# Kernel tuning notes

Measured on AMD Instinct MI355X. Metric: run time of the kernel, lower is better.

## Reference

```python
import jax, jax.numpy as jnp
import numpy as np

SCALE = 0.5

def setup_inputs() -> dict:
    key = jax.random.key(0)
    kx, kw, kb = jax.random.split(key, 3)
    N, Cin, H, W = 32, 64, 128, 128
    Cout, K = 128, 3
    x = jax.random.normal(kx, (N, Cin, H, W), dtype=jnp.float32)
    # kaiming_uniform with a=sqrt(5) -> bound = sqrt(3/fan_in) approx; uniform is fine for a reference
    fan_in = Cin * K * K
    bound = 1.0 / np.sqrt(fan_in)
    weight = jax.random.uniform(kw, (Cout, Cin, K, K), dtype=jnp.float32, minval=-bound, maxval=bound)
    bias = jax.random.uniform(kb, (Cout,), dtype=jnp.float32, minval=-bound, maxval=bound)
    return {"x": x, "weight": weight, "bias": bias}

def reference(x, weight, bias):
    # valid conv, stride 1: (N, Cout, OH, OW)
    y = jax.lax.conv_general_dilated(
        x, weight,
        window_strides=(1, 1),
        padding="VALID",
        dimension_numbers=("NCHW", "OIHW", "NCHW"),
    )
    y = (y + bias[None, :, None, None]) * SCALE
    # min over output channels, keepdim -> (N, 1, OH, OW)
    return jnp.min(y, axis=1, keepdims=True)
```

## Files before the change

kernel.cpp:

```cpp
#include <hip/hip_runtime.h>

constexpr int CN   = 32;
constexpr int CIN  = 64;
constexpr int CH   = 128;
constexpr int CW   = 128;
constexpr int COUT = 128;
constexpr int OHh  = 126;
constexpr int OWw  = 126;
constexpr int KTOT = 576;

typedef __attribute__((ext_vector_type(8))) short bf16x8;
typedef __attribute__((ext_vector_type(4))) float f32x4;

__device__ __forceinline__ unsigned short f2bf(float f) {
  union { float f; unsigned u; } v; v.f = f;
  unsigned u = v.u;
  u += 0x7FFFu + ((u >> 16) & 1u);
  return (unsigned short)(u >> 16);
}

__device__ __forceinline__ void gload_lds16(const unsigned short* g, unsigned short* l) {
  __builtin_amdgcn_global_load_lds(
      (const __attribute__((address_space(1))) unsigned int*)g,
      (__attribute__((address_space(3))) unsigned int*)l, 16, 0, 0);
}

__global__ __launch_bounds__(256) void prep_xt_kernel(const float* __restrict__ x,
                                                      unsigned short* __restrict__ xt) {
  __shared__ __align__(16) unsigned short s[128][72];
  const int b = blockIdx.x;
  const int n = b >> 7, h = b & 127;
  const float* src = x + (size_t)n * CIN * CH * CW + (size_t)h * CW;
  const int t = threadIdx.x;
  #pragma unroll
  for (int r = 0; r < 8; ++r) {
    int idx = r * 256 + t;
    int ci = idx >> 5, c0 = (idx & 31) << 2;
    float4 v = *(const float4*)(src + (size_t)ci * (CH * CW) + c0);
    s[c0 + 0][ci] = f2bf(v.x);
    s[c0 + 1][ci] = f2bf(v.y);
    s[c0 + 2][ci] = f2bf(v.z);
    s[c0 + 3][ci] = f2bf(v.w);
  }
  __syncthreads();
  unsigned short* dst = xt + (size_t)b * 8192;
  #pragma unroll
  for (int r = 0; r < 4; ++r) {
    int idx = r * 256 + t;
    int c = idx >> 3, sl = idx & 7;
    int half = sl >> 2, q = sl & 3;
    int lo = q ^ ((c >> 1) & 3);
    uint4 v = *(const uint4*)&s[c][half * 32 + lo * 8];
    *(uint4*)(dst + (size_t)c * 64 + sl * 8) = v;
  }
}

__global__ void prep_wt2_kernel(const float* __restrict__ w,
                                unsigned short* __restrict__ wt) {
  int i = blockIdx.x * 256 + threadIdx.x;
  if (i >= COUT * KTOT) return;
  int co = i / KTOT, k = i - co * KTOT;
  int kw = k / 192, r = k - kw * 192;
  int kh = r >> 6, q = r & 63;
  int half = q >> 5, qq = q & 31;
  int sl = qq >> 3, j = qq & 7;
  int o = sl ^ ((co >> 1) & 3);
  int ci = half * 32 + o * 8 + j;
  wt[i] = f2bf(w[co * 576 + ci * 9 + kh * 3 + kw]);
}

__global__ __launch_bounds__(512, 2)
void conv_min_mfma4(const unsigned short* __restrict__ xt,
                    const unsigned short* __restrict__ wt,
                    const float* __restrict__ bias,
                    float* __restrict__ out) {
  __shared__ __align__(16) unsigned short sX[2][4][132][32];
  __shared__ __align__(16) unsigned short sW[2][3][128][32];
  __shared__ float sRed[2][512];

  const int t   = threadIdx.x;
  const int bid = blockIdx.x;
  const int swz = (bid & 7) * 128 + (bid >> 3);
  const int n   = swz >> 5;
  const int oh0 = (swz & 31) * 4;

  const int lane = t & 63, w = t >> 6;
  const int wc = w & 1, wp = w >> 1;
  const int lg = lane >> 4, ln = lane & 15;

  const int xcq   = (t >> 2) * 64 + (t & 3) * 8;
  const int wco_o = (t >> 2) * 576 + (t & 3) * 8;

  const int chA = lg ^ ((ln >> 1) & 3);
  const char* Abase = (const char*)&sW[0][0][0][0] +
                      ((wc * 64 + ln) * 64 + chA * 16);
  const char* Bbase[3];
  #pragma unroll
  for (int kw = 0; kw < 3; ++kw) {
    int chB = lg ^ (((ln + kw) >> 1) & 3);
    Bbase[kw] = (const char*)&sX[0][0][0][0] +
                (wp * 8448 + (ln + kw) * 64 + chB * 16);
  }

  f32x4 acc[4][8];
  #pragma unroll
  for (int i = 0; i < 4; ++i)
    #pragma unroll
    for (int j = 0; j < 8; ++j)
      acc[i][j] = (f32x4){0.f, 0.f, 0.f, 0.f};

  auto stage = [&](int g, int bf) {
    const int kh = g >> 1, half = g & 1;
    unsigned short* ldsX = &sX[bf][0][0][0];
    unsigned short* ldsW = &sW[bf][0][0][0];
    #pragma unroll
    for (int r = 0; r < 4; ++r) {
      int h = oh0 + kh + r;
      h = h > 127 ? 127 : h;
      gload_lds16(xt + ((size_t)(n * 128 + h) << 13) + half * 32 + xcq,
                  ldsX + r * 4224 + w * 512);
    }
    const int wb = kh * 64 + half * 32;
    #pragma unroll
    for (int r = 0; r < 3; ++r)
      gload_lds16(wt + wb + wco_o + r * 192,
                  ldsW + r * 4096 + w * 512);
  };

  stage(0, 0);
  #pragma unroll
  for (int g = 0; g < 6; ++g) {
    const int bf = g & 1;
    if (g < 5) {
      stage(g + 1, bf ^ 1);
      __builtin_amdgcn_sched_barrier(0);
      asm volatile("s_waitcnt vmcnt(7)" ::: "memory");
    } else {
      asm volatile("s_waitcnt vmcnt(0)" ::: "memory");
    }
    __builtin_amdgcn_s_barrier();
    __builtin_amdgcn_sched_barrier(0);
    #pragma unroll
    for (int kw = 0; kw < 3; ++kw) {
      bf16x8 af[4], bfr[8];
      #pragma unroll
      for (int mi = 0; mi < 4; ++mi)
        af[mi] = *(const bf16x8*)(Abase + bf * 24576 + kw * 8192 + mi * 1024);
      #pragma unroll
      for (int ni = 0; ni < 8; ++ni)
        bfr[ni] = *(const bf16x8*)(Bbase[kw] + bf * 33792 + ni * 1024);
      #pragma unroll
      for (int mi = 0; mi < 4; ++mi)
        #pragma unroll
        for (int ni = 0; ni < 8; ++ni)
          acc[mi][ni] = __builtin_amdgcn_mfma_f32_16x16x32_bf16(
              af[mi], bfr[ni], acc[mi][ni], 0, 0, 0);
    }
    __builtin_amdgcn_s_barrier();
  }

  float bv[4][4];
  #pragma unroll
  for (int mi = 0; mi < 4; ++mi)
    #pragma unroll
    for (int r = 0; r < 4; ++r)
      bv[mi][r] = bias[wc * 64 + mi * 16 + lg * 4 + r];

  #pragma unroll
  for (int ni = 0; ni < 8; ++ni) {
    float m = 3.4e38f;
    #pragma unroll
    for (int mi = 0; mi < 4; ++mi)
      #pragma unroll
      for (int r = 0; r < 4; ++r)
        m = fminf(m, (acc[mi][ni][r] + bv[mi][r]) * 0.5f);
    m = fminf(m, __shfl_xor(m, 16));
    m = fminf(m, __shfl_xor(m, 32));
    if (lg == 0) sRed[wc][wp * 128 + ni * 16 + ln] = m;
  }
  __syncthreads();
  {
    int row = t >> 7, c = t & 127;
    if (c < OWw && oh0 + row < OHh)
      out[((size_t)n * OHh + oh0 + row) * OWw + c] = fminf(sRed[0][t], sRed[1][t]);
  }
}

__global__ void prep_wt_kernel(const float* __restrict__ w,
                               unsigned short* __restrict__ wt) {
  int i = blockIdx.x * 256 + threadIdx.x;
  if (i >= COUT * KTOT) return;
  int co = i / KTOT, kp = i - co * KTOT;
  int kw = kp / 192, rem = kp - kw * 192;
  int ci = rem / 3, kh = rem - ci * 3;
  wt[i] = f2bf(w[co * 576 + ci * 9 + kh * 3 + kw]);
}

template <bool USE_WT>
__global__ __launch_bounds__(256, 2)
void conv_min_fb(const float* __restrict__ x, const float* __restrict__ w,
                 const float* __restrict__ bias, const unsigned short* __restrict__ wt,
                 float* __restrict__ out) {
  __shared__ __align__(16) unsigned short sW[128][40];
  __shared__ __align__(16) unsigned short sX[128][40];
  __shared__ float sBias[COUT];
  __shared__ float sRed[2][128];
  const int t = threadIdx.x, bid = blockIdx.x;
  const int n = bid / OHh, oh = bid - n * OHh;
  if (t < COUT) sBias[t] = bias[t];
  const int hq = t & 7, q = t >> 3, c0 = q * 4;
  const int wco = t >> 1, whalf = t & 1;
  const int lane = t & 63, lg = lane >> 4, ln = lane & 15;
  const int wv = t >> 6, wc = wv & 1, wp = wv >> 1;
  f32x4 acc[4][4];
  #pragma unroll
  for (int i = 0; i < 4; ++i)
    #pragma unroll
    for (int j = 0; j < 4; ++j) acc[i][j] = (f32x4){0.f, 0.f, 0.f, 0.f};
  const float* xn = x + (size_t)n * CIN * CH * CW;
  for (int s = 0; s < 18; ++s) {
    const int k0 = s * 32;
    const int kw_s = s / 6;
    const int rembase = (s - kw_s * 6) * 32;
    float4 xa[2], xb[2]; int kkp[2];
    #pragma unroll
    for (int pi = 0; pi < 2; ++pi) {
      const int kk = 2 * hq + 16 * pi; kkp[pi] = kk;
      int rem0 = rembase + kk, ci0 = rem0 / 3, kh0 = rem0 - ci0 * 3;
      int rem1 = rem0 + 1, ci1 = rem1 / 3, kh1 = rem1 - ci1 * 3;
      xa[pi] = *(const float4*)(xn + (ci0 * CH + (oh + kh0)) * CW + c0);
      xb[pi] = *(const float4*)(xn + (ci1 * CH + (oh + kh1)) * CW + c0);
    }
    uint4 wv0, wv1;
    if constexpr (USE_WT) {
      const uint4* src = (const uint4*)(wt + wco * KTOT + k0 + whalf * 16);
      wv0 = src[0]; wv1 = src[1];
    } else {
      unsigned tmp[8];
      #pragma unroll
      for (int e = 0; e < 8; ++e) {
        int kk = whalf * 16 + 2 * e;
        int rem0 = rembase + kk, ci0 = rem0 / 3, kh0 = rem0 - ci0 * 3;
        int rem1 = rem0 + 1, ci1 = rem1 / 3, kh1 = rem1 - ci1 * 3;
        tmp[e] = (unsigned)f2bf(w[wco * 576 + ci0 * 9 + kh0 * 3 + kw_s]) |
                 ((unsigned)f2bf(w[wco * 576 + ci1 * 9 + kh1 * 3 + kw_s]) << 16);
      }
      wv0 = make_uint4(tmp[0], tmp[1], tmp[2], tmp[3]);
      wv1 = make_uint4(tmp[4], tmp[5], tmp[6], tmp[7]);
    }
    __syncthreads();
    #pragma unroll
    for (int pi = 0; pi < 2; ++pi)
      #pragma unroll
      for (int j = 0; j < 4; ++j) {
        int p = c0 + j - kw_s;
        unsigned pk = (unsigned)f2bf(((const float*)&xa[pi])[j]) |
                      ((unsigned)f2bf(((const float*)&xb[pi])[j]) << 16);
        if (p >= 0) *(unsigned*)&sX[p][kkp[pi]] = pk;
      }
    *(uint4*)&sW[wco][whalf * 16] = wv0;
    *(uint4*)&sW[wco][whalf * 16 + 8] = wv1;
    __syncthreads();
    bf16x8 af[4], bfr[4];
    #pragma unroll
    for (int mi = 0; mi < 4; ++mi) af[mi] = *(const bf16x8*)&sW[wc * 64 + mi * 16 + ln][lg * 8];
    #pragma unroll
    for (int ni = 0; ni < 4; ++ni) bfr[ni] = *(const bf16x8*)&sX[wp * 64 + ni * 16 + ln][lg * 8];
    #pragma unroll
    for (int mi = 0; mi < 4; ++mi)
      #pragma unroll
      for (int ni = 0; ni < 4; ++ni)
        acc[mi][ni] = __builtin_amdgcn_mfma_f32_16x16x32_bf16(af[mi], bfr[ni], acc[mi][ni], 0, 0, 0);
  }
  #pragma unroll
  for (int ni = 0; ni < 4; ++ni) {
    float m = 3.4e38f;
    #pragma unroll
    for (int mi = 0; mi < 4; ++mi)
      #pragma unroll
      for (int r = 0; r < 4; ++r)
        m = fminf(m, (acc[mi][ni][r] + sBias[wc * 64 + mi * 16 + lg * 4 + r]) * 0.5f);
    m = fminf(m, __shfl_xor(m, 16));
    m = fminf(m, __shfl_xor(m, 32));
    if (lg == 0) sRed[wc][wp * 64 + ni * 16 + ln] = m;
  }
  __syncthreads();
  if (t < OWw) out[(size_t)(n * OHh + oh) * OWw + t] = fminf(sRed[0][t], sRed[1][t]);
}

extern "C" void kernel_launch(void* const* d_in, const int* in_sizes, int n_in,
                              void* d_out, int out_size, void* d_ws, size_t ws_size,
                              hipStream_t stream) {
  const float* x    = (const float*)d_in[0];
  const float* w    = (const float*)d_in[1];
  const float* bias = (const float*)d_in[2];
  float* out = (float*)d_out;

  const size_t XT_BYTES = (size_t)CN * CH * CW * CIN * 2;
  const size_t WT_BYTES = (size_t)COUT * KTOT * 2;

  if (d_ws && ws_size >= XT_BYTES + WT_BYTES) {
    unsigned short* xt = (unsigned short*)d_ws;
    unsigned short* wt = (unsigned short*)((char*)d_ws + XT_BYTES);
    prep_xt_kernel<<<CN * CH, 256, 0, stream>>>(x, xt);
    prep_wt2_kernel<<<(COUT * KTOT + 255) / 256, 256, 0, stream>>>(w, wt);
    conv_min_mfma4<<<1024, 512, 0, stream>>>(xt, wt, bias, out);
  } else if (d_ws && ws_size >= WT_BYTES) {
    unsigned short* wt = (unsigned short*)d_ws;
    prep_wt_kernel<<<(COUT * KTOT + 255) / 256, 256, 0, stream>>>(w, wt);
    conv_min_fb<true><<<CN * OHh, 256, 0, stream>>>(x, w, bias, wt, out);
  } else {
    conv_min_fb<false><<<CN * OHh, 256, 0, stream>>>(x, w, bias, nullptr, out);
  }
}
```

Measured before the change: 104.5 us.

## Triple-buffer input tiles and interleave prefetch with per-kw MFMA phases

Stores the input tile in three LDS buffers with a prefetch distance of two stages, while weights stay double-buffered. Global-to-LDS loads are issued after the first fragment reads of each stage, and s_setprio brackets each MFMA block. The intent is to hide global load latency better behind matrix work. The cost is more LDS usage and barriers around every kw sub-step.

```diff
diff --git a/kernel.cpp b/kernel.cpp
--- a/kernel.cpp
+++ b/kernel.cpp
@@ -70,11 +70,11 @@
 }
 
 __global__ __launch_bounds__(512, 2)
-void conv_min_mfma4(const unsigned short* __restrict__ xt,
+void conv_min_mfma5(const unsigned short* __restrict__ xt,
                     const unsigned short* __restrict__ wt,
                     const float* __restrict__ bias,
                     float* __restrict__ out) {
-  __shared__ __align__(16) unsigned short sX[2][4][132][32];
+  __shared__ __align__(16) unsigned short sX[3][4][130][32];
   __shared__ __align__(16) unsigned short sW[2][3][128][32];
   __shared__ float sRed[2][512];
 
@@ -99,7 +99,7 @@
   for (int kw = 0; kw < 3; ++kw) {
     int chB = lg ^ (((ln + kw) >> 1) & 3);
     Bbase[kw] = (const char*)&sX[0][0][0][0] +
-                (wp * 8448 + (ln + kw) * 64 + chB * 16);
+                (wp * 8320 + (ln + kw) * 64 + chB * 16);
   }
 
   f32x4 acc[4][8];
@@ -109,54 +109,71 @@
     for (int j = 0; j < 8; ++j)
       acc[i][j] = (f32x4){0.f, 0.f, 0.f, 0.f};
 
-  auto stage = [&](int g, int bf) {
+  auto stageX = [&](int g) {
     const int kh = g >> 1, half = g & 1;
-    unsigned short* ldsX = &sX[bf][0][0][0];
-    unsigned short* ldsW = &sW[bf][0][0][0];
+    unsigned short* ldsX = &sX[g % 3][0][0][0];
     #pragma unroll
     for (int r = 0; r < 4; ++r) {
       int h = oh0 + kh + r;
       h = h > 127 ? 127 : h;
       gload_lds16(xt + ((size_t)(n * 128 + h) << 13) + half * 32 + xcq,
-                  ldsX + r * 4224 + w * 512);
+                  ldsX + r * 4160 + w * 512);
     }
+  };
+  auto stageW = [&](int g) {
+    const int kh = g >> 1, half = g & 1;
+    unsigned short* ldsW = &sW[g % 2][0][0][0];
     const int wb = kh * 64 + half * 32;
     #pragma unroll
     for (int r = 0; r < 3; ++r)
-      gload_lds16(wt + wb + wco_o + r * 192,
-                  ldsW + r * 4096 + w * 512);
+      gload_lds16(wt + wb + wco_o + r * 192, ldsW + r * 4096 + w * 512);
   };
 
-  stage(0, 0);
+  stageW(0);
+  stageX(0);
+  stageX(1);
+  asm volatile("s_waitcnt vmcnt(4)" ::: "memory");
+  __builtin_amdgcn_s_barrier();
+
   #pragma unroll
   for (int g = 0; g < 6; ++g) {
-    const int bf = g & 1;
-    if (g < 5) {
-      stage(g + 1, bf ^ 1);
-      __builtin_amdgcn_sched_barrier(0);
-      asm volatile("s_waitcnt vmcnt(7)" ::: "memory");
-    } else {
-      asm volatile("s_waitcnt vmcnt(0)" ::: "memory");
-    }
-    __builtin_amdgcn_s_barrier();
-    __builtin_amdgcn_sched_barrier(0);
+    const int xb = g % 3, wb2 = g & 1;
     #pragma unroll
     for (int kw = 0; kw < 3; ++kw) {
       bf16x8 af[4], bfr[8];
+      const char* bA = Abase + wb2 * 24576 + kw * 8192;
+      const char* bB = Bbase[kw] + xb * 33280;
       #pragma unroll
       for (int mi = 0; mi < 4; ++mi)
-        af[mi] = *(const bf16x8*)(Abase + bf * 24576 + kw * 8192 + mi * 1024);
+        af[mi] = *(const bf16x8*)(bA + mi * 1024);
       #pragma unroll
       for (int ni = 0; ni < 8; ++ni)
-        bfr[ni] = *(const bf16x8*)(Bbase[kw] + bf * 33792 + ni * 1024);
+        bfr[ni] = *(const bf16x8*)(bB + ni * 1024);
+
+      if (kw == 0) {
+        if (g <= 4) stageW(g + 1);
+        if (g <= 3) stageX(g + 2);
+      }
+      if (kw == 2) {
+        if (g <= 3)      asm volatile("s_waitcnt vmcnt(4)" ::: "memory");
+        else if (g == 4) asm volatile("s_waitcnt vmcnt(0)" ::: "memory");
+      }
+
+      __builtin_amdgcn_s_barrier();
+      asm volatile("s_waitcnt lgkmcnt(0)" ::: "memory");
+      __builtin_amdgcn_sched_barrier(0);
+      __builtin_amdgcn_s_setprio(1);
       #pragma unroll
       for (int mi = 0; mi < 4; ++mi)
         #pragma unroll
         for (int ni = 0; ni < 8; ++ni)
           acc[mi][ni] = __builtin_amdgcn_mfma_f32_16x16x32_bf16(
               af[mi], bfr[ni], acc[mi][ni], 0, 0, 0);
+      __builtin_amdgcn_s_setprio(0);
+      __builtin_amdgcn_s_barrier();
+      if (kw == 2)
+        __builtin_amdgcn_sched_barrier(0);
     }
-    __builtin_amdgcn_s_barrier();
   }
 
   float bv[4][4];
@@ -304,7 +321,7 @@
     unsigned short* wt = (unsigned short*)((char*)d_ws + XT_BYTES);
     prep_xt_kernel<<<CN * CH, 256, 0, stream>>>(x, xt);
     prep_wt2_kernel<<<(COUT * KTOT + 255) / 256, 256, 0, stream>>>(w, wt);
-    conv_min_mfma4<<<1024, 512, 0, stream>>>(xt, wt, bias, out);
+    conv_min_mfma5<<<1024, 512, 0, stream>>>(xt, wt, bias, out);
   } else if (d_ws && ws_size >= WT_BYTES) {
     unsigned short* wt = (unsigned short*)d_ws;
     prep_wt_kernel<<<(COUT * KTOT + 255) / 256, 256, 0, stream>>>(w, wt);
```

New measurement: 111.4 us. +6.5%, slower.

## Load weights from global in MFMA fragment order, shrink tiles, raise occupancy

Applied to the files above, without the earlier changes.

Weights are now pre-permuted on the device into a per-lane MFMA fragment layout and read straight from global/L2 into registers, so the weight LDS buffer and its staging go away. Each block covers 2 output rows instead of 4, across 2016 blocks, and each wave holds a 4x4 accumulator tile instead of 4x8. This lowers register and LDS use so launch bounds can ask for 4 blocks per CU. The K loop becomes 18 steps with a barrier only every third step, and s_setprio is raised around the MFMA bursts. The trade-off is that weight fragments are re-read from cache by every wave, and the smaller tiles give less reuse of the input data.

```diff
diff --git a/kernel.cpp b/kernel.cpp
--- a/kernel.cpp
+++ b/kernel.cpp
@@ -55,108 +55,91 @@
   }
 }
 
-__global__ void prep_wt2_kernel(const float* __restrict__ w,
-                                unsigned short* __restrict__ wt) {
-  int i = blockIdx.x * 256 + threadIdx.x;
-  if (i >= COUT * KTOT) return;
-  int co = i / KTOT, k = i - co * KTOT;
-  int kw = k / 192, r = k - kw * 192;
-  int kh = r >> 6, q = r & 63;
-  int half = q >> 5, qq = q & 31;
-  int sl = qq >> 3, j = qq & 7;
-  int o = sl ^ ((co >> 1) & 3);
-  int ci = half * 32 + o * 8 + j;
-  wt[i] = f2bf(w[co * 576 + ci * 9 + kh * 3 + kw]);
-}
-
-__global__ __launch_bounds__(512, 2)
-void conv_min_mfma4(const unsigned short* __restrict__ xt,
-                    const unsigned short* __restrict__ wt,
+__global__ void prep_wt3_kernel(const float* __restrict__ w,
+                                unsigned short* __restrict__ wt3) {
+  int e = blockIdx.x * 256 + threadIdx.x;
+  if (e >= COUT * KTOT) return;
+  int j = e & 7, lane = (e >> 3) & 63, mi = (e >> 9) & 3, wc = (e >> 11) & 1;
+  int p = e >> 12;
+  int G = p / 3, kw = p - G * 3;
+  int kh = G >> 1, half = G & 1;
+  int co = wc * 64 + mi * 16 + (lane & 15);
+  int ci = half * 32 + (lane >> 4) * 8 + j;
+  wt3[e] = f2bf(w[co * 576 + ci * 9 + kh * 3 + kw]);
+}
+
+__global__ __launch_bounds__(512, 4)
+void conv_min_mfma6(const unsigned short* __restrict__ xt,
+                    const unsigned short* __restrict__ wt3,
                     const float* __restrict__ bias,
                     float* __restrict__ out) {
-  __shared__ __align__(16) unsigned short sX[2][4][132][32];
-  __shared__ __align__(16) unsigned short sW[2][3][128][32];
-  __shared__ float sRed[2][512];
+  __shared__ __align__(16) unsigned short sX[2][2][130][32];
+  __shared__ float sRed[2][256];
 
   const int t   = threadIdx.x;
   const int bid = blockIdx.x;
-  const int swz = (bid & 7) * 128 + (bid >> 3);
-  const int n   = swz >> 5;
-  const int oh0 = (swz & 31) * 4;
+  const int swz = (bid & 7) * 252 + (bid >> 3);
+  const int n   = swz / 63;
+  const int oh0 = (swz - n * 63) * 2;
 
   const int lane = t & 63, w = t >> 6;
-  const int wc = w & 1, wp = w >> 1;
+  const int wc = w & 1;
+  const int wr = (w >> 1) & 1;
+  const int wh = w >> 2;
   const int lg = lane >> 4, ln = lane & 15;
 
-  const int xcq   = (t >> 2) * 64 + (t & 3) * 8;
-  const int wco_o = (t >> 2) * 576 + (t & 3) * 8;
-
-  const int chA = lg ^ ((ln >> 1) & 3);
-  const char* Abase = (const char*)&sW[0][0][0][0] +
-                      ((wc * 64 + ln) * 64 + chA * 16);
-  const char* Bbase[3];
+  const int xcq = (t >> 2) * 64 + (t & 3) * 8;
+
+  const char* Bb[3];
   #pragma unroll
   for (int kw = 0; kw < 3; ++kw) {
-    int chB = lg ^ (((ln + kw) >> 1) & 3);
-    Bbase[kw] = (const char*)&sX[0][0][0][0] +
-                (wp * 8448 + (ln + kw) * 64 + chB * 16);
-  }
-
-  f32x4 acc[4][8];
+    int row = wh * 64 + ln + kw;
+    int ch = lg ^ ((row >> 1) & 3);
+    Bb[kw] = (const char*)&sX[0][0][0][0] + wr * 8320 + row * 64 + ch * 16;
+  }
+  const unsigned short* wlane = wt3 + wc * 2048 + lane * 8;
+
+  f32x4 acc[4][4];
   #pragma unroll
   for (int i = 0; i < 4; ++i)
     #pragma unroll
-    for (int j = 0; j < 8; ++j)
+    for (int j = 0; j < 4; ++j)
       acc[i][j] = (f32x4){0.f, 0.f, 0.f, 0.f};
 
-  auto stage = [&](int g, int bf) {
-    const int kh = g >> 1, half = g & 1;
-    unsigned short* ldsX = &sX[bf][0][0][0];
-    unsigned short* ldsW = &sW[bf][0][0][0];
-    #pragma unroll
-    for (int r = 0; r < 4; ++r) {
-      int h = oh0 + kh + r;
-      h = h > 127 ? 127 : h;
-      gload_lds16(xt + ((size_t)(n * 128 + h) << 13) + half * 32 + xcq,
-                  ldsX + r * 4224 + w * 512);
-    }
-    const int wb = kh * 64 + half * 32;
-    #pragma unroll
-    for (int r = 0; r < 3; ++r)
-      gload_lds16(wt + wb + wco_o + r * 192,
-                  ldsW + r * 4096 + w * 512);
+  auto stageX = [&](int G, int buf) {
+    #pragma unroll
+    for (int r = 0; r < 2; ++r) {
+      int h = oh0 + (G >> 1) + r;
+      gload_lds16(xt + ((size_t)(n * 128 + h) << 13) + (G & 1) * 32 + xcq,
+                  &sX[buf][r][0][0] + w * 512);
+    }
   };
 
-  stage(0, 0);
-  #pragma unroll
-  for (int g = 0; g < 6; ++g) {
-    const int bf = g & 1;
-    if (g < 5) {
-      stage(g + 1, bf ^ 1);
-      __builtin_amdgcn_sched_barrier(0);
-      asm volatile("s_waitcnt vmcnt(7)" ::: "memory");
-    } else {
+  stageX(0, 0);
+
+  #pragma unroll
+  for (int p = 0; p < 18; ++p) {
+    const int G = p / 3, kw = p - G * 3, buf = G & 1;
+    if (kw == 0) {
       asm volatile("s_waitcnt vmcnt(0)" ::: "memory");
-    }
-    __builtin_amdgcn_s_barrier();
-    __builtin_amdgcn_sched_barrier(0);
-    #pragma unroll
-    for (int kw = 0; kw < 3; ++kw) {
-      bf16x8 af[4], bfr[8];
-      #pragma unroll
-      for (int mi = 0; mi < 4; ++mi)
-        af[mi] = *(const bf16x8*)(Abase + bf * 24576 + kw * 8192 + mi * 1024);
-      #pragma unroll
-      for (int ni = 0; ni < 8; ++ni)
-        bfr[ni] = *(const bf16x8*)(Bbase[kw] + bf * 33792 + ni * 1024);
-      #pragma unroll
-      for (int mi = 0; mi < 4; ++mi)
-        #pragma unroll
-        for (int ni = 0; ni < 8; ++ni)
-          acc[mi][ni] = __builtin_amdgcn_mfma_f32_16x16x32_bf16(
-              af[mi], bfr[ni], acc[mi][ni], 0, 0, 0);
-    }
-    __builtin_amdgcn_s_barrier();
+      __builtin_amdgcn_s_barrier();
+      if (G < 5) stageX(G + 1, buf ^ 1);
+    }
+    bf16x8 af[4], bfr[4];
+    #pragma unroll
+    for (int mi = 0; mi < 4; ++mi)
+      af[mi] = *(const bf16x8*)(wlane + p * 4096 + mi * 512);
+    #pragma unroll
+    for (int ni = 0; ni < 4; ++ni)
+      bfr[ni] = *(const bf16x8*)(Bb[kw] + buf * 16640 + ni * 1024);
+    __builtin_amdgcn_s_setprio(1);
+    #pragma unroll
+    for (int mi = 0; mi < 4; ++mi)
+      #pragma unroll
+      for (int ni = 0; ni < 4; ++ni)
+        acc[mi][ni] = __builtin_amdgcn_mfma_f32_16x16x32_bf16(
+            af[mi], bfr[ni], acc[mi][ni], 0, 0, 0);
+    __builtin_amdgcn_s_setprio(0);
   }
 
   float bv[4][4];
@@ -167,7 +150,7 @@
       bv[mi][r] = bias[wc * 64 + mi * 16 + lg * 4 + r];
 
   #pragma unroll
-  for (int ni = 0; ni < 8; ++ni) {
+  for (int ni = 0; ni < 4; ++ni) {
     float m = 3.4e38f;
     #pragma unroll
     for (int mi = 0; mi < 4; ++mi)
@@ -176,12 +159,12 @@
         m = fminf(m, (acc[mi][ni][r] + bv[mi][r]) * 0.5f);
     m = fminf(m, __shfl_xor(m, 16));
     m = fminf(m, __shfl_xor(m, 32));
-    if (lg == 0) sRed[wc][wp * 128 + ni * 16 + ln] = m;
+    if (lg == 0) sRed[wc][wr * 128 + wh * 64 + ni * 16 + ln] = m;
   }
   __syncthreads();
-  {
+  if (t < 256) {
     int row = t >> 7, c = t & 127;
-    if (c < OWw && oh0 + row < OHh)
+    if (c < OWw)
       out[((size_t)n * OHh + oh0 + row) * OWw + c] = fminf(sRed[0][t], sRed[1][t]);
   }
 }
@@ -300,11 +283,11 @@
   const size_t WT_BYTES = (size_t)COUT * KTOT * 2;
 
   if (d_ws && ws_size >= XT_BYTES + WT_BYTES) {
-    unsigned short* xt = (unsigned short*)d_ws;
-    unsigned short* wt = (unsigned short*)((char*)d_ws + XT_BYTES);
+    unsigned short* xt  = (unsigned short*)d_ws;
+    unsigned short* wt3 = (unsigned short*)((char*)d_ws + XT_BYTES);
     prep_xt_kernel<<<CN * CH, 256, 0, stream>>>(x, xt);
-    prep_wt2_kernel<<<(COUT * KTOT + 255) / 256, 256, 0, stream>>>(w, wt);
-    conv_min_mfma4<<<1024, 512, 0, stream>>>(xt, wt, bias, out);
+    prep_wt3_kernel<<<(COUT * KTOT + 255) / 256, 256, 0, stream>>>(w, wt3);
+    conv_min_mfma6<<<2016, 512, 0, stream>>>(xt, wt3, bias, out);
   } else if (d_ws && ws_size >= WT_BYTES) {
     unsigned short* wt = (unsigned short*)d_ws;
     prep_wt_kernel<<<(COUT * KTOT + 255) / 256, 256, 0, stream>>>(w, wt);
```

New measurement: 104.1 us. About the same (-0.4%).
